# Kernel tuning notes

Hardware: AMD Instinct MI355X
Metric: run time of the kernel (lower is better)

## Reference

```python
import jax, jax.numpy as jnp
import numpy as np

OUT_H, OUT_W = 512, 512
BATCH, CHANNELS = 64, 3


def setup_inputs() -> dict:
    key = jax.random.key(0)
    k1, k2 = jax.random.split(key)
    U = jax.random.normal(k1, (BATCH, OUT_H, OUT_W, CHANNELS), dtype=jnp.float32)
    theta = jax.random.normal(k2, (BATCH, 1), dtype=jnp.float32)
    return {"U": U, "theta": theta}


def reference(U, theta):
    B = U.shape[0]
    H, W = OUT_H, OUT_W
    # normalized sampling grid [H*W, 3] with homogeneous coordinate
    gx, gy = jnp.meshgrid(jnp.linspace(-1.0, 1.0, W), jnp.linspace(-1.0, 1.0, H))
    grid = jnp.stack([gx, gy, jnp.ones_like(gx)], axis=-1).reshape(H * W, 3)
    # rotation-only affine matrix [B, 2, 3]
    cos_t, sin_t, z = jnp.cos(theta), jnp.sin(theta), jnp.zeros_like(theta)
    rot = jnp.concatenate([cos_t, -sin_t, z, sin_t, cos_t, z], axis=1).reshape(B, 2, 3)
    # transformed source coords [B, H*W, 2]
    T_g = jnp.einsum('bij,nj->bni', rot, grid)
    x = (T_g[..., 0] + 1.0) * (W - 1) / 2.0
    y = (T_g[..., 1] + 1.0) * (H - 1) / 2.0
    x0f = jnp.floor(x).astype(jnp.int32)
    y0f = jnp.floor(y).astype(jnp.int32)
    x0 = jnp.clip(x0f, 0, W - 1)
    x1 = jnp.clip(x0f + 1, 0, W - 1)
    y0 = jnp.clip(y0f, 0, H - 1)
    y1 = jnp.clip(y0f + 1, 0, H - 1)
    # 4-corner gathers, batched: [B, H*W, C]
    gather = jax.vmap(lambda u, yy, xx: u[yy, xx])
    Ia = gather(U, y0, x0)
    Ib = gather(U, y1, x0)
    Ic = gather(U, y0, x1)
    Id = gather(U, y1, x1)
    x0_f, x1_f = x0.astype(jnp.float32), x1.astype(jnp.float32)
    y0_f, y1_f = y0.astype(jnp.float32), y1.astype(jnp.float32)
    wa = (x1_f - x) * (y1_f - y)
    wb = (x1_f - x) * (y - y0_f)
    wc = (x - x0_f) * (y1_f - y)
    wd = (x - x0_f) * (y - y0_f)
    out = (wa[..., None] * Ia + wb[..., None] * Ib
           + wc[..., None] * Ic + wd[..., None] * Id)
    return out.reshape(B, H, W, -1)
```

## Files before the change

kernel.cpp:

```cpp
#include <hip/hip_runtime.h>

#define OUT_H 512
#define OUT_W 512
#define BATCH 64
#define CHANS 3

#define LROWS 47
#define LROW_F4 37
#define LROW_DW 148

__global__ __launch_bounds__(256) void st_bilinear_kernel(
    const float* __restrict__ U,
    const float* __restrict__ theta,
    float* __restrict__ out)
{
    __shared__ float4 smem4[LROWS * LROW_F4];

    int blk  = blockIdx.x;
    int lblk = (blk & 7) * 2048 + (blk >> 3);

    int b  = lblk >> 8;
    int t  = lblk & 255;
    int i0 = (t >> 4) << 5;
    int j0 = (t & 15) << 5;

    int tid = threadIdx.x;

    float tt = theta[b];
    float s, c;
    __sincosf(tt, &s, &c);

    const float scale = 2.0f / 511.0f;
    float gx0 = (float)j0 * scale - 1.0f;
    float gy0 = (float)i0 * scale - 1.0f;
    float xb0 = (c * gx0 - s * gy0 + 1.0f) * 255.5f;
    float yb0 = (s * gx0 + c * gy0 + 1.0f) * 255.5f;

    float xmin = xb0 + fminf(0.0f, 31.0f * c) + fminf(0.0f, -31.0f * s);
    float ymin = yb0 + fminf(0.0f, 31.0f * s) + fminf(0.0f,  31.0f * c);

    int bx0 = min(max((int)floorf(xmin), 0), OUT_W - 1);
    int by0 = min(max((int)floorf(ymin), 0), OUT_H - 1);
    int bx_load = min(bx0, OUT_W - 48);
    int by_load = min(by0, OUT_H - 46);

    const float* Ub = U + (size_t)b * (OUT_H * OUT_W * CHANS);
    const float* gbase = Ub + (size_t)by_load * (OUT_W * CHANS) + bx_load * CHANS;
    for (int u = tid; u < 46 * 36; u += 256) {
        int r  = u / 36;
        int c4 = u - r * 36;
        float4 v = *(const float4*)(gbase + (size_t)r * (OUT_W * CHANS) + c4 * 4);
        smem4[r * LROW_F4 + c4] = v;
    }
    __syncthreads();

    const float* lds = (const float*)smem4;

    int jl = tid & 31;
    int il_base = tid >> 5;
#pragma unroll
    for (int k = 0; k < 4; ++k) {
        int il = (k << 3) + il_base;
        float x = xb0 + c * (float)jl - s * (float)il;
        float y = yb0 + s * (float)jl + c * (float)il;

        float x0f = floorf(x);
        float y0f = floorf(y);
        float fx = x - x0f;
        float fy = y - y0f;
        float hx1 = 1.0f - fx;
        float hy1 = 1.0f - fy;
        float wa = hx1 * hy1;
        float wb = hx1 * fy;
        float wc = fx * hy1;
        float wd = fx * fy;

        int x0c = min(max((int)x0f, 0), OUT_W - 1);
        int y0c = min(max((int)y0f, 0), OUT_H - 1);
        int lx = x0c - bx_load;
        int ly = y0c - by_load;

        const float* lp = lds + ly * LROW_DW + lx * CHANS;
        float v00_0 = lp[0],   v01_0 = lp[3];
        float v00_1 = lp[1],   v01_1 = lp[4];
        float v00_2 = lp[2],   v01_2 = lp[5];
        float v10_0 = lp[LROW_DW + 0], v11_0 = lp[LROW_DW + 3];
        float v10_1 = lp[LROW_DW + 1], v11_1 = lp[LROW_DW + 4];
        float v10_2 = lp[LROW_DW + 2], v11_2 = lp[LROW_DW + 5];

        float r0 = wa * v00_0 + wc * v01_0 + wb * v10_0 + wd * v11_0;
        float r1 = wa * v00_1 + wc * v01_1 + wb * v10_1 + wd * v11_1;
        float r2 = wa * v00_2 + wc * v01_2 + wb * v10_2 + wd * v11_2;

        bool valid = (x >= 0.0f) && (x < 511.0f) && (y >= 0.0f) && (y < 511.0f);
        r0 = valid ? r0 : 0.0f;
        r1 = valid ? r1 : 0.0f;
        r2 = valid ? r2 : 0.0f;

        float* po = out + (((size_t)b * OUT_H + (i0 + il)) * OUT_W + (j0 + jl)) * CHANS;
        po[0] = r0;
        po[1] = r1;
        po[2] = r2;
    }
}

extern "C" void kernel_launch(void* const* d_in, const int* in_sizes, int n_in,
                              void* d_out, int out_size, void* d_ws, size_t ws_size,
                              hipStream_t stream) {
    const float* U     = (const float*)d_in[0];
    const float* theta = (const float*)d_in[1];
    float* out = (float*)d_out;

    int blocks = BATCH * (OUT_H / 32) * (OUT_W / 32);
    st_bilinear_kernel<<<blocks, 256, 0, stream>>>(U, theta, out);
}
```

Baseline: 105.6 us.

## Stage tile in LDS as fp16 pixels and vectorize four-pixel float4 stores

Converts each staged source pixel to packed half precision (8 bytes per pixel, padded pitch) so each bilinear corner needs one 64-bit LDS read, and does the interpolation with packed half2 FMAs. Each thread now computes four consecutive output pixels along a row and writes them as three float4 stores instead of scalar stores. This cuts LDS read instructions and global store transactions, at the cost of fp16 rounding of inputs and weights, which may exceed the accuracy tolerance. Global loads become float2+float pairs per pixel instead of float4.

```diff
diff --git a/kernel.cpp b/kernel.cpp
--- a/kernel.cpp
+++ b/kernel.cpp
@@ -1,4 +1,5 @@
 #include <hip/hip_runtime.h>
+#include <hip/hip_fp16.h>
 
 #define OUT_H 512
 #define OUT_W 512
@@ -6,15 +7,14 @@
 #define CHANS 3
 
 #define LROWS 47
-#define LROW_F4 37
-#define LROW_DW 148
+#define LPITCH 49
 
 __global__ __launch_bounds__(256) void st_bilinear_kernel(
     const float* __restrict__ U,
     const float* __restrict__ theta,
     float* __restrict__ out)
 {
-    __shared__ float4 smem4[LROWS * LROW_F4];
+    __shared__ uint2 sm[LROWS * LPITCH + 1];
 
     int blk  = blockIdx.x;
     int lblk = (blk & 7) * 2048 + (blk >> 3);
@@ -45,63 +45,79 @@
     int by_load = min(by0, OUT_H - 46);
 
     const float* Ub = U + (size_t)b * (OUT_H * OUT_W * CHANS);
-    const float* gbase = Ub + (size_t)by_load * (OUT_W * CHANS) + bx_load * CHANS;
-    for (int u = tid; u < 46 * 36; u += 256) {
-        int r  = u / 36;
-        int c4 = u - r * 36;
-        float4 v = *(const float4*)(gbase + (size_t)r * (OUT_W * CHANS) + c4 * 4);
-        smem4[r * LROW_F4 + c4] = v;
+    const float* gb = Ub + ((size_t)by_load * OUT_W + bx_load) * CHANS;
+    for (int u = tid; u < 46 * 48; u += 256) {
+        int r  = u / 48;
+        int px = u - r * 48;
+        const float* p = gb + (size_t)r * (OUT_W * CHANS) + px * CHANS;
+        float2 c01 = *(const float2*)p;
+        float  c2  = p[2];
+        __half2 h01 = __floats2half2_rn(c01.x, c01.y);
+        __half2 h2  = __floats2half2_rn(c2, 0.0f);
+        uint2 v;
+        v.x = *(const unsigned int*)&h01;
+        v.y = *(const unsigned int*)&h2;
+        sm[r * LPITCH + px] = v;
     }
     __syncthreads();
 
-    const float* lds = (const float*)smem4;
+    int il = tid >> 3;
+    int jb = (tid & 7) << 2;
+    float ilf = (float)il;
+    float xr = xb0 - s * ilf;
+    float yr = yb0 + c * ilf;
 
-    int jl = tid & 31;
-    int il_base = tid >> 5;
+    float o[12];
 #pragma unroll
-    for (int k = 0; k < 4; ++k) {
-        int il = (k << 3) + il_base;
-        float x = xb0 + c * (float)jl - s * (float)il;
-        float y = yb0 + s * (float)jl + c * (float)il;
+    for (int p = 0; p < 4; ++p) {
+        float jlf = (float)(jb + p);
+        float x = fmaf(c, jlf, xr);
+        float y = fmaf(s, jlf, yr);
 
         float x0f = floorf(x);
         float y0f = floorf(y);
         float fx = x - x0f;
         float fy = y - y0f;
-        float hx1 = 1.0f - fx;
-        float hy1 = 1.0f - fy;
-        float wa = hx1 * hy1;
-        float wb = hx1 * fy;
-        float wc = fx * hy1;
-        float wd = fx * fy;
+        float hx = 1.0f - fx;
+        float hy = 1.0f - fy;
+        __half2 wa2 = __float2half2_rn(hx * hy);
+        __half2 wb2 = __float2half2_rn(hx * fy);
+        __half2 wc2 = __float2half2_rn(fx * hy);
+        __half2 wd2 = __float2half2_rn(fx * fy);
 
-        int x0c = min(max((int)x0f, 0), OUT_W - 1);
-        int y0c = min(max((int)y0f, 0), OUT_H - 1);
-        int lx = x0c - bx_load;
-        int ly = y0c - by_load;
+        int lx = min(max((int)x0f - bx_load, 0), 48);
+        int ly = min(max((int)y0f - by_load, 0), 45);
+        int idx = ly * LPITCH + lx;
 
-        const float* lp = lds + ly * LROW_DW + lx * CHANS;
-        float v00_0 = lp[0],   v01_0 = lp[3];
-        float v00_1 = lp[1],   v01_1 = lp[4];
-        float v00_2 = lp[2],   v01_2 = lp[5];
-        float v10_0 = lp[LROW_DW + 0], v11_0 = lp[LROW_DW + 3];
-        float v10_1 = lp[LROW_DW + 1], v11_1 = lp[LROW_DW + 4];
-        float v10_2 = lp[LROW_DW + 2], v11_2 = lp[LROW_DW + 5];
+        uint2 rA = sm[idx];
+        uint2 rC = sm[idx + 1];
+        uint2 rB = sm[idx + LPITCH];
+        uint2 rD = sm[idx + LPITCH + 1];
 
-        float r0 = wa * v00_0 + wc * v01_0 + wb * v10_0 + wd * v11_0;
-        float r1 = wa * v00_1 + wc * v01_1 + wb * v10_1 + wd * v11_1;
-        float r2 = wa * v00_2 + wc * v01_2 + wb * v10_2 + wd * v11_2;
+        __half2 a01 = *(const __half2*)&rA.x, a2 = *(const __half2*)&rA.y;
+        __half2 c01 = *(const __half2*)&rC.x, c2 = *(const __half2*)&rC.y;
+        __half2 b01 = *(const __half2*)&rB.x, b2 = *(const __half2*)&rB.y;
+        __half2 d01 = *(const __half2*)&rD.x, d2 = *(const __half2*)&rD.y;
+
+        __half2 r01 = __hmul2(wa2, a01);
+        r01 = __hfma2(wb2, b01, r01);
+        r01 = __hfma2(wc2, c01, r01);
+        r01 = __hfma2(wd2, d01, r01);
+        __half2 r2h = __hmul2(wa2, a2);
+        r2h = __hfma2(wb2, b2, r2h);
+        r2h = __hfma2(wc2, c2, r2h);
+        r2h = __hfma2(wd2, d2, r2h);
 
         bool valid = (x >= 0.0f) && (x < 511.0f) && (y >= 0.0f) && (y < 511.0f);
-        r0 = valid ? r0 : 0.0f;
-        r1 = valid ? r1 : 0.0f;
-        r2 = valid ? r2 : 0.0f;
+        o[p * 3 + 0] = valid ? __low2float(r01)  : 0.0f;
+        o[p * 3 + 1] = valid ? __high2float(r01) : 0.0f;
+        o[p * 3 + 2] = valid ? __low2float(r2h)  : 0.0f;
+    }
 
-        float* po = out + (((size_t)b * OUT_H + (i0 + il)) * OUT_W + (j0 + jl)) * CHANS;
-        po[0] = r0;
-        po[1] = r1;
-        po[2] = r2;
-    }
+    float* po = out + (((size_t)b * OUT_H + (i0 + il)) * OUT_W + (j0 + jb)) * CHANS;
+    ((float4*)po)[0] = make_float4(o[0], o[1], o[2],  o[3]);
+    ((float4*)po)[1] = make_float4(o[4], o[5], o[6],  o[7]);
+    ((float4*)po)[2] = make_float4(o[8], o[9], o[10], o[11]);
 }
 
 extern "C" void kernel_launch(void* const* d_in, const int* in_sizes, int n_in,
```

Result: slower. 117.3 us (+11.1%).
